# Kernel optimization log

Hardware: AMD Instinct MI355X
Metric: run time of the kernel (lower is better)

Reference implementation:

```python
import jax, jax.numpy as jnp
import numpy as np

H = 512          # hidden_size
SH = 120         # scoring_net_hidden_size
B = 1024         # batch
S = 64           # num_sentences


def setup_inputs() -> dict:
    key = jax.random.key(0)
    ks = jax.random.split(key, 12)
    sc = 0.05
    return {
        "C": jax.random.normal(ks[0], (B, S, H), jnp.float32),
        "Q": jax.random.normal(ks[1], (B, 1, H), jnp.float32),
        "prev_M": jax.random.normal(ks[2], (B, 1, H), jnp.float32),
        # scoring network params: fc1: 4H -> SH, fc2: SH -> 1
        "fc1_w": jax.random.normal(ks[3], (SH, 4 * H), jnp.float32) * sc,
        "fc1_b": jnp.zeros((SH,), jnp.float32),
        "fc2_w": jax.random.normal(ks[4], (1, SH), jnp.float32) * sc,
        "fc2_b": jnp.zeros((1,), jnp.float32),
        # GRU params (torch layout: rows ordered r, z, n)
        "W_ih": jax.random.normal(ks[5], (3 * H, H), jnp.float32) * sc,
        "W_hh": jax.random.normal(ks[6], (3 * H, H), jnp.float32) * sc,
        "b_ih": jnp.zeros((3 * H,), jnp.float32),
        "b_hh": jnp.zeros((3 * H,), jnp.float32),
    }


def reference(C, Q, prev_M, fc1_w, fc1_b, fc2_w, fc2_b, W_ih, W_hh, b_ih, b_hh):
    # --- scoring network (arch=1 feature vector) ---
    feat = jnp.concatenate(
        [C * Q, C * prev_M, jnp.abs(C - Q), jnp.abs(C - prev_M)], axis=2
    )  # [B, S, 4H]
    h1 = jnp.tanh(jnp.einsum("bsf,kf->bsk", feat, fc1_w) + fc1_b)
    G = jax.nn.sigmoid((jnp.einsum("bsk,ok->bso", h1, fc2_w) + fc2_b)[..., 0])  # [B, S]

    # --- gated GRU memory update over sentences ---
    xg_all = jnp.einsum("bsh,gh->bsg", C, W_ih) + b_ih  # [B, S, 3H] precomputed input gates

    def step(h, inp):
        xg, g = inp  # xg: [B, 3H], g: [B]
        hg = h @ W_hh.T + b_hh
        xr, xz, xn = jnp.split(xg, 3, axis=-1)
        hr, hz, hn = jnp.split(hg, 3, axis=-1)
        r = jax.nn.sigmoid(xr + hr)
        z = jax.nn.sigmoid(xz + hz)
        n = jnp.tanh(xn + r * hn)
        h_gru = (1.0 - z) * n + z * h          # standard torch GRU update
        g = g[:, None]
        h_new = g * h_gru + (1.0 - g) * h      # episodic gating
        return h_new, None

    h0 = jnp.zeros((C.shape[0], H), C.dtype)
    h_final, _ = jax.lax.scan(step, h0, (xg_all.transpose(1, 0, 2), G.T))
    return h_final[:, None, :]  # [B, 1, H]
```

## Files before the change

### kernel.cpp

```cpp
#include <hip/hip_runtime.h>
#include <hip/hip_bf16.h>

#define H_ 512
#define SH_ 120
#define B_ 1024
#define S_ 64

typedef __bf16 bf16x8 __attribute__((ext_vector_type(8)));
typedef float floatx4 __attribute__((ext_vector_type(4)));

__device__ __forceinline__ float bf2f(ushort u) {
    union { unsigned int i; float f; } v; v.i = ((unsigned int)u) << 16; return v.f;
}
__device__ __forceinline__ ushort f2bf(float f) {
    union { float f; unsigned int i; } v; v.f = f;
    unsigned int x = v.i;
    unsigned int r = (x + 0x7fffu + ((x >> 16) & 1u)) >> 16;
    return (ushort)r;
}

__global__ __launch_bounds__(256) void prep_w(
    const float* __restrict__ fc1w, ushort* __restrict__ fc1wb,
    const float* __restrict__ Wih,  ushort* __restrict__ Wihb,
    const float* __restrict__ Whh,  ushort* __restrict__ Whhb)
{
    const int stride = gridDim.x * blockDim.x;
    const int tid = blockIdx.x * blockDim.x + threadIdx.x;
    for (int i = tid; i < 61440; i += stride) {
        const float4 v = ((const float4*)fc1w)[i];
        ushort4 o; o.x = f2bf(v.x); o.y = f2bf(v.y); o.z = f2bf(v.z); o.w = f2bf(v.w);
        ((ushort4*)fc1wb)[i] = o;
    }
    for (int i = tid; i < 196608; i += stride) {
        const float4 v = ((const float4*)Wih)[i];
        ushort4 o; o.x = f2bf(v.x); o.y = f2bf(v.y); o.z = f2bf(v.z); o.w = f2bf(v.w);
        ((ushort4*)Wihb)[i] = o;
    }
    for (int i = tid; i < 196608; i += stride) {
        const float4 v = ((const float4*)Whh)[i];
        ushort4 o; o.x = f2bf(v.x); o.y = f2bf(v.y); o.z = f2bf(v.z); o.w = f2bf(v.w);
        ((ushort4*)Whhb)[i] = o;
    }
}

__global__ __launch_bounds__(256) void g_kernel(
    const float* __restrict__ C, const float* __restrict__ Q,
    const float* __restrict__ M, const ushort* __restrict__ fc1wb,
    const float* __restrict__ fc1b, const float* __restrict__ fc2w,
    const float* __restrict__ fc2b, float* __restrict__ G)
{
    __shared__ float qrow[H_];
    __shared__ float mrow[H_];
    __shared__ __align__(16) ushort featT[64 * 72];
    __shared__ __align__(16) ushort wT[128 * 72];
    __shared__ float h1s[64 * 132];

    const int b = blockIdx.x;
    const int t = threadIdx.x;
    for (int i = t; i < H_; i += 256) { qrow[i] = Q[(size_t)b * H_ + i]; mrow[i] = M[(size_t)b * H_ + i]; }

    const int wrow = t >> 1;
    const int wc0  = (t & 1) * 32;
    if (wrow >= SH_) {
        uint4* dst = (uint4*)&wT[wrow * 72 + wc0];
        const uint4 z = {0u, 0u, 0u, 0u};
        dst[0] = z; dst[1] = z; dst[2] = z; dst[3] = z;
    }
    __syncthreads();

    const int lane = t & 63;
    const int wv   = t >> 6;
    const int quad = lane >> 4;
    const int l15  = lane & 15;
    const int arow = wv * 16 + l15;
    const int s    = t >> 2;
    const int c0   = (t & 3) * 16;

    floatx4 acc[8];
#pragma unroll
    for (int i = 0; i < 8; ++i) acc[i] = (floatx4){0.f, 0.f, 0.f, 0.f};

    for (int hc = 0; hc < H_; hc += 64) {
        float cr[16];
        {
            const float4* csrc = (const float4*)(C + ((size_t)b * S_ + s) * H_ + hc + c0);
            *(float4*)&cr[0]  = csrc[0];
            *(float4*)&cr[4]  = csrc[1];
            *(float4*)&cr[8]  = csrc[2];
            *(float4*)&cr[12] = csrc[3];
        }
#pragma unroll
        for (int seg = 0; seg < 4; ++seg) {
#pragma unroll
            for (int u = 0; u < 16; ++u) {
                const int kk = c0 + u;
                const float c = cr[u];
                const float o = (seg == 0 || seg == 2) ? qrow[hc + kk] : mrow[hc + kk];
                const float v = (seg < 2) ? c * o : fabsf(c - o);
                featT[s * 72 + kk] = f2bf(v);
            }
            if (wrow < SH_) {
                const uint4* src = (const uint4*)(fc1wb + (size_t)wrow * (4 * H_) + seg * H_ + hc + wc0);
                uint4* dst = (uint4*)&wT[wrow * 72 + wc0];
                dst[0] = src[0]; dst[1] = src[1]; dst[2] = src[2]; dst[3] = src[3];
            }
            __syncthreads();
#pragma unroll
            for (int ks = 0; ks < 64; ks += 32) {
                const int ao = ks + quad * 8;
                const bf16x8 af = *(const bf16x8*)&featT[arow * 72 + ao];
#pragma unroll
                for (int nt = 0; nt < 8; ++nt) {
                    const bf16x8 bfr = *(const bf16x8*)&wT[(nt * 16 + l15) * 72 + ao];
                    acc[nt] = __builtin_amdgcn_mfma_f32_16x16x32_bf16(af, bfr, acc[nt], 0, 0, 0);
                }
            }
            __syncthreads();
        }
    }

#pragma unroll
    for (int nt = 0; nt < 8; ++nt) {
        const int col = nt * 16 + l15;
        const float bias = (col < SH_) ? fc1b[col] : 0.f;
#pragma unroll
        for (int r = 0; r < 4; ++r) {
            const int row = wv * 16 + quad * 4 + r;
            h1s[row * 132 + col] = (col < SH_) ? tanhf(acc[nt][r] + bias) : 0.f;
        }
    }
    __syncthreads();
    {
        const int part = t & 3;
        float sum = 0.f;
        for (int k = part; k < SH_; k += 4) sum += h1s[s * 132 + k] * fc2w[k];
        sum += __shfl_xor(sum, 1);
        sum += __shfl_xor(sum, 2);
        if (part == 0) {
            const float logit = sum + fc2b[0];
            G[(size_t)b * S_ + s] = 1.f / (1.f + expf(-logit));
        }
    }
}

__global__ __launch_bounds__(256) void scan_step(
    const float* __restrict__ C, const ushort* __restrict__ Wihb,
    const ushort* __restrict__ Whhb, const float* __restrict__ bih,
    const float* __restrict__ bhh, const float* __restrict__ G,
    const ushort* __restrict__ hhi_r, const ushort* __restrict__ hlo_r,
    ushort* __restrict__ hhi_w, ushort* __restrict__ hlo_w,
    float* __restrict__ out, int tstep, int last)
{
    __shared__ __align__(16) ushort As[3 * 4608];
    __shared__ __align__(16) ushort Bs[2 * 6912];

    const int bx = blockIdx.x;
    const int jt = bx & 15;
    const int bt = bx >> 4;
    const int jb = jt * 32;
    const int bb = bt * 64;
    const int t  = threadIdx.x;
    const int lane = t & 63;
    const int wv   = t >> 6;
    const int quad = lane >> 4;
    const int l15  = lane & 15;
    const int arow = wv * 16 + l15;
    const int crow = t >> 2;
    const int cc0  = (t & 3) * 16;

    floatx4 acc_r[2], acc_z[2], acc_xn[2], acc_hn[2];
#pragma unroll
    for (int i = 0; i < 2; ++i) {
        acc_r[i] = (floatx4){0.f,0.f,0.f,0.f}; acc_z[i]  = (floatx4){0.f,0.f,0.f,0.f};
        acc_xn[i]= (floatx4){0.f,0.f,0.f,0.f}; acc_hn[i] = (floatx4){0.f,0.f,0.f,0.f};
    }

    for (int kc = 0; kc < H_; kc += 64) {
        {
            const float4* src = (const float4*)(C + ((size_t)(bb + crow) * S_ + tstep) * H_ + kc + cc0);
            float cr[16];
            *(float4*)&cr[0]  = src[0];
            *(float4*)&cr[4]  = src[1];
            *(float4*)&cr[8]  = src[2];
            *(float4*)&cr[12] = src[3];
            __align__(16) ushort cb[16];
#pragma unroll
            for (int u = 0; u < 16; ++u) cb[u] = f2bf(cr[u]);
            uint4* d = (uint4*)&As[crow * 72 + cc0];
            d[0] = ((uint4*)cb)[0]; d[1] = ((uint4*)cb)[1];
        }
#pragma unroll
        for (int i = 0; i < 4; ++i) {
            const int gid  = i * 256 + t;
            const int tile = gid >> 9;
            const int rem  = gid & 511;
            const int row  = rem >> 3;
            const int grp  = rem & 7;
            const ushort* src = (tile ? hlo_r : hhi_r) + (size_t)(bb + row) * H_ + kc + grp * 8;
            *(uint4*)&As[(1 + tile) * 4608 + row * 72 + grp * 8] = *(const uint4*)src;
        }
#pragma unroll
        for (int i = 0; i < 6; ++i) {
            const int gid = i * 256 + t;
            const int mat = (gid >= 768) ? 1 : 0;
            const int rem = gid - mat * 768;
            const int row = rem >> 3;
            const int grp = rem & 7;
            const int gate = row >> 5;
            const int jj   = row & 31;
            const int grow = gate * H_ + jb + jj;
            const ushort* src = (mat ? Whhb : Wihb) + (size_t)grow * H_ + kc + grp * 8;
            *(uint4*)&Bs[mat * 6912 + row * 72 + grp * 8] = *(const uint4*)src;
        }
        __syncthreads();
#pragma unroll
        for (int ks = 0; ks < 64; ks += 32) {
            const int ao = ks + quad * 8;
            const bf16x8 a_c  = *(const bf16x8*)&As[0 * 4608 + arow * 72 + ao];
            const bf16x8 a_hh = *(const bf16x8*)&As[1 * 4608 + arow * 72 + ao];
            const bf16x8 a_hl = *(const bf16x8*)&As[2 * 4608 + arow * 72 + ao];
#pragma unroll
            for (int nt = 0; nt < 2; ++nt) {
                const int jj = nt * 16 + l15;
                const bf16x8 ih_r = *(const bf16x8*)&Bs[0 * 6912 + (0 * 32 + jj) * 72 + ao];
                const bf16x8 ih_z = *(const bf16x8*)&Bs[0 * 6912 + (1 * 32 + jj) * 72 + ao];
                const bf16x8 ih_n = *(const bf16x8*)&Bs[0 * 6912 + (2 * 32 + jj) * 72 + ao];
                const bf16x8 hh_r = *(const bf16x8*)&Bs[1 * 6912 + (0 * 32 + jj) * 72 + ao];
                const bf16x8 hh_z = *(const bf16x8*)&Bs[1 * 6912 + (1 * 32 + jj) * 72 + ao];
                const bf16x8 hh_n = *(const bf16x8*)&Bs[1 * 6912 + (2 * 32 + jj) * 72 + ao];
                acc_r[nt]  = __builtin_amdgcn_mfma_f32_16x16x32_bf16(a_c,  ih_r, acc_r[nt],  0, 0, 0);
                acc_r[nt]  = __builtin_amdgcn_mfma_f32_16x16x32_bf16(a_hh, hh_r, acc_r[nt],  0, 0, 0);
                acc_r[nt]  = __builtin_amdgcn_mfma_f32_16x16x32_bf16(a_hl, hh_r, acc_r[nt],  0, 0, 0);
                acc_z[nt]  = __builtin_amdgcn_mfma_f32_16x16x32_bf16(a_c,  ih_z, acc_z[nt],  0, 0, 0);
                acc_z[nt]  = __builtin_amdgcn_mfma_f32_16x16x32_bf16(a_hh, hh_z, acc_z[nt],  0, 0, 0);
                acc_z[nt]  = __builtin_amdgcn_mfma_f32_16x16x32_bf16(a_hl, hh_z, acc_z[nt],  0, 0, 0);
                acc_xn[nt] = __builtin_amdgcn_mfma_f32_16x16x32_bf16(a_c,  ih_n, acc_xn[nt], 0, 0, 0);
                acc_hn[nt] = __builtin_amdgcn_mfma_f32_16x16x32_bf16(a_hh, hh_n, acc_hn[nt], 0, 0, 0);
                acc_hn[nt] = __builtin_amdgcn_mfma_f32_16x16x32_bf16(a_hl, hh_n, acc_hn[nt], 0, 0, 0);
            }
        }
        __syncthreads();
    }

#pragma unroll
    for (int nt = 0; nt < 2; ++nt) {
        const int j = jb + nt * 16 + l15;
        const float br  = bih[j]          + bhh[j];
        const float bz  = bih[H_ + j]     + bhh[H_ + j];
        const float bxn = bih[2 * H_ + j];
        const float bhn = bhh[2 * H_ + j];
#pragma unroll
        for (int r4 = 0; r4 < 4; ++r4) {
            const int b = bb + wv * 16 + quad * 4 + r4;
            const size_t idx = (size_t)b * H_ + j;
            const float hold = bf2f(hhi_r[idx]) + bf2f(hlo_r[idx]);
            const float g = G[(size_t)b * S_ + tstep];
            const float rg = 1.f / (1.f + expf(-(acc_r[nt][r4] + br)));
            const float zg = 1.f / (1.f + expf(-(acc_z[nt][r4] + bz)));
            const float ng = tanhf(acc_xn[nt][r4] + bxn + rg * (acc_hn[nt][r4] + bhn));
            const float hgru = (1.f - zg) * ng + zg * hold;
            const float hnew = g * hgru + (1.f - g) * hold;
            const ushort hb = f2bf(hnew);
            hhi_w[idx] = hb;
            hlo_w[idx] = f2bf(hnew - bf2f(hb));
            if (last) out[idx] = hnew;
        }
    }
}

extern "C" void kernel_launch(void* const* d_in, const int* in_sizes, int n_in,
                              void* d_out, int out_size, void* d_ws, size_t ws_size,
                              hipStream_t stream) {
    (void)in_sizes; (void)n_in; (void)out_size; (void)ws_size;
    const float* C    = (const float*)d_in[0];
    const float* Q    = (const float*)d_in[1];
    const float* M    = (const float*)d_in[2];
    const float* fc1w = (const float*)d_in[3];
    const float* fc1b = (const float*)d_in[4];
    const float* fc2w = (const float*)d_in[5];
    const float* fc2b = (const float*)d_in[6];
    const float* Wih  = (const float*)d_in[7];
    const float* Whh  = (const float*)d_in[8];
    const float* bih  = (const float*)d_in[9];
    const float* bhh  = (const float*)d_in[10];
    float* out = (float*)d_out;

    char* ws = (char*)d_ws;
    float*  Gbuf  = (float*)ws;
    ushort* hhi0  = (ushort*)(ws + 262144);
    ushort* hlo0  = (ushort*)(ws + 262144 + 1048576);
    ushort* hhi1  = (ushort*)(ws + 262144 + 2097152);
    ushort* hlo1  = (ushort*)(ws + 262144 + 3145728);
    ushort* fc1wb = (ushort*)(ws + 4456448);
    ushort* Wihb  = (ushort*)(ws + 4947968);
    ushort* Whhb  = (ushort*)(ws + 6520832);

    hipMemsetAsync(hhi0, 0, 2097152, stream);

    prep_w<<<256, 256, 0, stream>>>(fc1w, fc1wb, Wih, Wihb, Whh, Whhb);
    g_kernel<<<B_, 256, 0, stream>>>(C, Q, M, fc1wb, fc1b, fc2w, fc2b, Gbuf);
    for (int t = 0; t < S_; ++t) {
        const ushort* hr_hi = (t & 1) ? hhi1 : hhi0;
        const ushort* hr_lo = (t & 1) ? hlo1 : hlo0;
        ushort* hw_hi = (t & 1) ? hhi0 : hhi1;
        ushort* hw_lo = (t & 1) ? hlo0 : hlo1;
        scan_step<<<256, 256, 0, stream>>>(C, Wihb, Whhb, bih, bhh, Gbuf,
                                           hr_hi, hr_lo, hw_hi, hw_lo,
                                           out, t, (t == S_ - 1) ? 1 : 0);
    }
}
```

Baseline: 1.462 ms.

## Hoist input-gate GEMM out of scan into chunked batched xg kernel

The input projection C·W_ih moves out of each per-step scan kernel into a separate batched GEMM kernel. That kernel computes bf16 xg for 8 timesteps at a time using 128x256 tiles with double-buffered LDS. The scan step now only does the recurrent W_hh matmul over the split-precision hidden state, with register-prefetched double buffering, and reads the precomputed xg from a workspace buffer. This removes the redundant per-step W_ih loads and small-tile inefficiency, but adds xg global traffic, an extra bf16 rounding of the input gates, and 8 more launches.

```diff
diff --git a/kernel.cpp b/kernel.cpp
--- a/kernel.cpp
+++ b/kernel.cpp
@@ -17,6 +17,10 @@
     unsigned int x = v.i;
     unsigned int r = (x + 0x7fffu + ((x >> 16) & 1u)) >> 16;
     return (ushort)r;
+}
+__device__ __forceinline__ ushort f2bf_fast(float f) {
+    __bf16 b = (__bf16)f;
+    union { __bf16 b; ushort u; } v; v.b = b; return v.u;
 }
 
 __global__ __launch_bounds__(256) void prep_w(
@@ -143,16 +147,111 @@
     }
 }
 
-__global__ __launch_bounds__(256) void scan_step(
+__global__ __launch_bounds__(256, 1) void xg_kernel(
     const float* __restrict__ C, const ushort* __restrict__ Wihb,
-    const ushort* __restrict__ Whhb, const float* __restrict__ bih,
-    const float* __restrict__ bhh, const float* __restrict__ G,
+    ushort* __restrict__ xg, int c)
+{
+    __shared__ __align__(16) ushort As[2][128 * 72];
+    __shared__ __align__(16) ushort Bs[2][256 * 72];
+
+    const int bx = blockIdx.x;
+    const int mt = bx & 63;
+    const int ntile = bx >> 6;
+    const int t = threadIdx.x;
+    const int lane = t & 63;
+    const int wv   = t >> 6;
+    const int quad = lane >> 4;
+    const int l15  = lane & 15;
+
+    const int ar = t >> 1;
+    const int ah = (t & 1) * 32;
+    const int grow = mt * 128 + ar;
+    const float* aptr = C + ((size_t)(grow >> 3) * S_ + c * 8 + (grow & 7)) * H_ + ah;
+    const ushort* bptr = Wihb + (size_t)(ntile * 256 + t) * H_;
+
+    floatx4 acc[2][16];
+#pragma unroll
+    for (int i = 0; i < 2; ++i)
+#pragma unroll
+        for (int j = 0; j < 16; ++j) acc[i][j] = (floatx4){0.f, 0.f, 0.f, 0.f};
+
+    {
+        float av[32];
+#pragma unroll
+        for (int q = 0; q < 8; ++q) *(float4*)&av[q * 4] = *(const float4*)(aptr + q * 4);
+        __align__(16) ushort ab[32];
+#pragma unroll
+        for (int u = 0; u < 32; ++u) ab[u] = f2bf_fast(av[u]);
+        uint4* dst = (uint4*)&As[0][ar * 72 + ah];
+        dst[0] = ((uint4*)ab)[0]; dst[1] = ((uint4*)ab)[1];
+        dst[2] = ((uint4*)ab)[2]; dst[3] = ((uint4*)ab)[3];
+#pragma unroll
+        for (int g = 0; g < 8; ++g)
+            *(uint4*)&Bs[0][t * 72 + g * 8] = *(const uint4*)(bptr + g * 8);
+    }
+    __syncthreads();
+
+    for (int kci = 0; kci < 8; ++kci) {
+        const int cur = kci & 1;
+        float av[32]; uint4 bv[8];
+        if (kci < 7) {
+            const int kn = (kci + 1) * 64;
+#pragma unroll
+            for (int q = 0; q < 8; ++q) *(float4*)&av[q * 4] = *(const float4*)(aptr + kn + q * 4);
+#pragma unroll
+            for (int g = 0; g < 8; ++g) bv[g] = *(const uint4*)(bptr + kn + g * 8);
+        }
+#pragma unroll
+        for (int ks = 0; ks < 64; ks += 32) {
+            const int ao = ks + quad * 8;
+            const bf16x8 a0 = *(const bf16x8*)&As[cur][(wv * 32 + l15) * 72 + ao];
+            const bf16x8 a1 = *(const bf16x8*)&As[cur][(wv * 32 + 16 + l15) * 72 + ao];
+#pragma unroll
+            for (int nf = 0; nf < 16; ++nf) {
+                const bf16x8 bfr = *(const bf16x8*)&Bs[cur][(nf * 16 + l15) * 72 + ao];
+                acc[0][nf] = __builtin_amdgcn_mfma_f32_16x16x32_bf16(a0, bfr, acc[0][nf], 0, 0, 0);
+                acc[1][nf] = __builtin_amdgcn_mfma_f32_16x16x32_bf16(a1, bfr, acc[1][nf], 0, 0, 0);
+            }
+        }
+        if (kci < 7) {
+            __align__(16) ushort ab[32];
+#pragma unroll
+            for (int u = 0; u < 32; ++u) ab[u] = f2bf_fast(av[u]);
+            uint4* dst = (uint4*)&As[cur ^ 1][ar * 72 + ah];
+            dst[0] = ((uint4*)ab)[0]; dst[1] = ((uint4*)ab)[1];
+            dst[2] = ((uint4*)ab)[2]; dst[3] = ((uint4*)ab)[3];
+#pragma unroll
+            for (int g = 0; g < 8; ++g)
+                *(uint4*)&Bs[cur ^ 1][t * 72 + g * 8] = bv[g];
+        }
+        __syncthreads();
+    }
+
+#pragma unroll
+    for (int mf = 0; mf < 2; ++mf) {
+#pragma unroll
+        for (int nf = 0; nf < 16; ++nf) {
+            const int n = ntile * 256 + nf * 16 + l15;
+#pragma unroll
+            for (int r = 0; r < 4; ++r) {
+                const int row = mt * 128 + wv * 32 + mf * 16 + quad * 4 + r;
+                xg[(size_t)row * 1536 + n] = f2bf(acc[mf][nf][r]);
+            }
+        }
+    }
+}
+
+__global__ __launch_bounds__(256, 1) void scan_step(
+    const ushort* __restrict__ xg, const ushort* __restrict__ Whhb,
+    const float* __restrict__ bih, const float* __restrict__ bhh,
+    const float* __restrict__ G,
     const ushort* __restrict__ hhi_r, const ushort* __restrict__ hlo_r,
     ushort* __restrict__ hhi_w, ushort* __restrict__ hlo_w,
-    float* __restrict__ out, int tstep, int last)
+    float* __restrict__ out, int tstep, int sl, int last)
 {
-    __shared__ __align__(16) ushort As[3 * 4608];
-    __shared__ __align__(16) ushort Bs[2 * 6912];
+    __shared__ __align__(16) ushort Hs[2][2 * 4608];
+    __shared__ __align__(16) ushort Ws[2][6912];
+    __shared__ __align__(16) ushort xgs[64 * 96];
 
     const int bx = blockIdx.x;
     const int jt = bx & 15;
@@ -165,30 +264,25 @@
     const int quad = lane >> 4;
     const int l15  = lane & 15;
     const int arow = wv * 16 + l15;
-    const int crow = t >> 2;
-    const int cc0  = (t & 3) * 16;
-
-    floatx4 acc_r[2], acc_z[2], acc_xn[2], acc_hn[2];
+
+    floatx4 acc_r[2], acc_z[2], acc_xn2[2], acc_hn[2];
 #pragma unroll
     for (int i = 0; i < 2; ++i) {
-        acc_r[i] = (floatx4){0.f,0.f,0.f,0.f}; acc_z[i]  = (floatx4){0.f,0.f,0.f,0.f};
-        acc_xn[i]= (floatx4){0.f,0.f,0.f,0.f}; acc_hn[i] = (floatx4){0.f,0.f,0.f,0.f};
-    }
-
-    for (int kc = 0; kc < H_; kc += 64) {
-        {
-            const float4* src = (const float4*)(C + ((size_t)(bb + crow) * S_ + tstep) * H_ + kc + cc0);
-            float cr[16];
-            *(float4*)&cr[0]  = src[0];
-            *(float4*)&cr[4]  = src[1];
-            *(float4*)&cr[8]  = src[2];
-            *(float4*)&cr[12] = src[3];
-            __align__(16) ushort cb[16];
-#pragma unroll
-            for (int u = 0; u < 16; ++u) cb[u] = f2bf(cr[u]);
-            uint4* d = (uint4*)&As[crow * 72 + cc0];
-            d[0] = ((uint4*)cb)[0]; d[1] = ((uint4*)cb)[1];
-        }
+        acc_r[i] = (floatx4){0.f,0.f,0.f,0.f}; acc_z[i]   = (floatx4){0.f,0.f,0.f,0.f};
+        acc_xn2[i]=(floatx4){0.f,0.f,0.f,0.f}; acc_hn[i]  = (floatx4){0.f,0.f,0.f,0.f};
+    }
+
+#pragma unroll
+    for (int i = 0; i < 3; ++i) {
+        const int gid  = i * 256 + t;
+        const int seg  = gid >> 2;
+        const int q    = gid & 3;
+        const int row  = seg / 3;
+        const int gate = seg - row * 3;
+        const ushort* src = xg + ((size_t)(bb + row) * 8 + sl) * 1536 + gate * H_ + jb + q * 8;
+        *(uint4*)&xgs[row * 96 + gate * 32 + q * 8] = *(const uint4*)src;
+    }
+    {
 #pragma unroll
         for (int i = 0; i < 4; ++i) {
             const int gid  = i * 256 + t;
@@ -196,47 +290,83 @@
             const int rem  = gid & 511;
             const int row  = rem >> 3;
             const int grp  = rem & 7;
-            const ushort* src = (tile ? hlo_r : hhi_r) + (size_t)(bb + row) * H_ + kc + grp * 8;
-            *(uint4*)&As[(1 + tile) * 4608 + row * 72 + grp * 8] = *(const uint4*)src;
-        }
-#pragma unroll
-        for (int i = 0; i < 6; ++i) {
+            const ushort* src = (tile ? hlo_r : hhi_r) + (size_t)(bb + row) * H_ + grp * 8;
+            *(uint4*)&Hs[0][tile * 4608 + row * 72 + grp * 8] = *(const uint4*)src;
+        }
+#pragma unroll
+        for (int i = 0; i < 3; ++i) {
             const int gid = i * 256 + t;
-            const int mat = (gid >= 768) ? 1 : 0;
-            const int rem = gid - mat * 768;
-            const int row = rem >> 3;
-            const int grp = rem & 7;
+            const int row = gid >> 3;
+            const int grp = gid & 7;
             const int gate = row >> 5;
             const int jj   = row & 31;
-            const int grow = gate * H_ + jb + jj;
-            const ushort* src = (mat ? Whhb : Wihb) + (size_t)grow * H_ + kc + grp * 8;
-            *(uint4*)&Bs[mat * 6912 + row * 72 + grp * 8] = *(const uint4*)src;
-        }
-        __syncthreads();
+            const ushort* src = Whhb + (size_t)(gate * H_ + jb + jj) * H_ + grp * 8;
+            *(uint4*)&Ws[0][row * 72 + grp * 8] = *(const uint4*)src;
+        }
+    }
+    __syncthreads();
+
+    for (int kci = 0; kci < 8; ++kci) {
+        const int cur = kci & 1;
+        uint4 hv[4], wvr[3];
+        if (kci < 7) {
+            const int kn = (kci + 1) * 64;
+#pragma unroll
+            for (int i = 0; i < 4; ++i) {
+                const int gid  = i * 256 + t;
+                const int tile = gid >> 9;
+                const int rem  = gid & 511;
+                const int row  = rem >> 3;
+                const int grp  = rem & 7;
+                const ushort* src = (tile ? hlo_r : hhi_r) + (size_t)(bb + row) * H_ + kn + grp * 8;
+                hv[i] = *(const uint4*)src;
+            }
+#pragma unroll
+            for (int i = 0; i < 3; ++i) {
+                const int gid = i * 256 + t;
+                const int row = gid >> 3;
+                const int grp = gid & 7;
+                const int gate = row >> 5;
+                const int jj   = row & 31;
+                wvr[i] = *(const uint4*)(Whhb + (size_t)(gate * H_ + jb + jj) * H_ + kn + grp * 8);
+            }
+        }
 #pragma unroll
         for (int ks = 0; ks < 64; ks += 32) {
             const int ao = ks + quad * 8;
-            const bf16x8 a_c  = *(const bf16x8*)&As[0 * 4608 + arow * 72 + ao];
-            const bf16x8 a_hh = *(const bf16x8*)&As[1 * 4608 + arow * 72 + ao];
-            const bf16x8 a_hl = *(const bf16x8*)&As[2 * 4608 + arow * 72 + ao];
+            const bf16x8 a_hh = *(const bf16x8*)&Hs[cur][arow * 72 + ao];
+            const bf16x8 a_hl = *(const bf16x8*)&Hs[cur][4608 + arow * 72 + ao];
 #pragma unroll
             for (int nt = 0; nt < 2; ++nt) {
                 const int jj = nt * 16 + l15;
-                const bf16x8 ih_r = *(const bf16x8*)&Bs[0 * 6912 + (0 * 32 + jj) * 72 + ao];
-                const bf16x8 ih_z = *(const bf16x8*)&Bs[0 * 6912 + (1 * 32 + jj) * 72 + ao];
-                const bf16x8 ih_n = *(const bf16x8*)&Bs[0 * 6912 + (2 * 32 + jj) * 72 + ao];
-                const bf16x8 hh_r = *(const bf16x8*)&Bs[1 * 6912 + (0 * 32 + jj) * 72 + ao];
-                const bf16x8 hh_z = *(const bf16x8*)&Bs[1 * 6912 + (1 * 32 + jj) * 72 + ao];
-                const bf16x8 hh_n = *(const bf16x8*)&Bs[1 * 6912 + (2 * 32 + jj) * 72 + ao];
-                acc_r[nt]  = __builtin_amdgcn_mfma_f32_16x16x32_bf16(a_c,  ih_r, acc_r[nt],  0, 0, 0);
-                acc_r[nt]  = __builtin_amdgcn_mfma_f32_16x16x32_bf16(a_hh, hh_r, acc_r[nt],  0, 0, 0);
-                acc_r[nt]  = __builtin_amdgcn_mfma_f32_16x16x32_bf16(a_hl, hh_r, acc_r[nt],  0, 0, 0);
-                acc_z[nt]  = __builtin_amdgcn_mfma_f32_16x16x32_bf16(a_c,  ih_z, acc_z[nt],  0, 0, 0);
-                acc_z[nt]  = __builtin_amdgcn_mfma_f32_16x16x32_bf16(a_hh, hh_z, acc_z[nt],  0, 0, 0);
-                acc_z[nt]  = __builtin_amdgcn_mfma_f32_16x16x32_bf16(a_hl, hh_z, acc_z[nt],  0, 0, 0);
-                acc_xn[nt] = __builtin_amdgcn_mfma_f32_16x16x32_bf16(a_c,  ih_n, acc_xn[nt], 0, 0, 0);
-                acc_hn[nt] = __builtin_amdgcn_mfma_f32_16x16x32_bf16(a_hh, hh_n, acc_hn[nt], 0, 0, 0);
-                acc_hn[nt] = __builtin_amdgcn_mfma_f32_16x16x32_bf16(a_hl, hh_n, acc_hn[nt], 0, 0, 0);
+                const bf16x8 w_r = *(const bf16x8*)&Ws[cur][(0 * 32 + jj) * 72 + ao];
+                const bf16x8 w_z = *(const bf16x8*)&Ws[cur][(1 * 32 + jj) * 72 + ao];
+                const bf16x8 w_n = *(const bf16x8*)&Ws[cur][(2 * 32 + jj) * 72 + ao];
+                acc_r[nt]  = __builtin_amdgcn_mfma_f32_16x16x32_bf16(a_hh, w_r, acc_r[nt],  0, 0, 0);
+                acc_r[nt]  = __builtin_amdgcn_mfma_f32_16x16x32_bf16(a_hl, w_r, acc_r[nt],  0, 0, 0);
+                acc_z[nt]  = __builtin_amdgcn_mfma_f32_16x16x32_bf16(a_hh, w_z, acc_z[nt],  0, 0, 0);
+                acc_z[nt]  = __builtin_amdgcn_mfma_f32_16x16x32_bf16(a_hl, w_z, acc_z[nt],  0, 0, 0);
+                acc_hn[nt] = __builtin_amdgcn_mfma_f32_16x16x32_bf16(a_hh, w_n, acc_hn[nt], 0, 0, 0);
+                acc_hn[nt] = __builtin_amdgcn_mfma_f32_16x16x32_bf16(a_hl, w_n, acc_hn[nt], 0, 0, 0);
+            }
+        }
+        if (kci < 7) {
+            const int cn = cur ^ 1;
+#pragma unroll
+            for (int i = 0; i < 4; ++i) {
+                const int gid  = i * 256 + t;
+                const int tile = gid >> 9;
+                const int rem  = gid & 511;
+                const int row  = rem >> 3;
+                const int grp  = rem & 7;
+                *(uint4*)&Hs[cn][tile * 4608 + row * 72 + grp * 8] = hv[i];
+            }
+#pragma unroll
+            for (int i = 0; i < 3; ++i) {
+                const int gid = i * 256 + t;
+                const int row = gid >> 3;
+                const int grp = gid & 7;
+                *(uint4*)&Ws[cn][row * 72 + grp * 8] = wvr[i];
             }
         }
         __syncthreads();
@@ -244,20 +374,25 @@
 
 #pragma unroll
     for (int nt = 0; nt < 2; ++nt) {
-        const int j = jb + nt * 16 + l15;
+        const int jc = nt * 16 + l15;
+        const int j  = jb + jc;
         const float br  = bih[j]          + bhh[j];
         const float bz  = bih[H_ + j]     + bhh[H_ + j];
         const float bxn = bih[2 * H_ + j];
         const float bhn = bhh[2 * H_ + j];
 #pragma unroll
         for (int r4 = 0; r4 < 4; ++r4) {
-            const int b = bb + wv * 16 + quad * 4 + r4;
+            const int bl = wv * 16 + quad * 4 + r4;
+            const int b  = bb + bl;
             const size_t idx = (size_t)b * H_ + j;
+            const float xr = bf2f(xgs[bl * 96 + 0 * 32 + jc]);
+            const float xz = bf2f(xgs[bl * 96 + 1 * 32 + jc]);
+            const float xn = bf2f(xgs[bl * 96 + 2 * 32 + jc]);
             const float hold = bf2f(hhi_r[idx]) + bf2f(hlo_r[idx]);
             const float g = G[(size_t)b * S_ + tstep];
-            const float rg = 1.f / (1.f + expf(-(acc_r[nt][r4] + br)));
-            const float zg = 1.f / (1.f + expf(-(acc_z[nt][r4] + bz)));
-            const float ng = tanhf(acc_xn[nt][r4] + bxn + rg * (acc_hn[nt][r4] + bhn));
+            const float rg = 1.f / (1.f + expf(-(acc_r[nt][r4] + xr + br)));
+            const float zg = 1.f / (1.f + expf(-(acc_z[nt][r4] + xz + bz)));
+            const float ng = tanhf(xn + bxn + rg * (acc_hn[nt][r4] + bhn));
             const float hgru = (1.f - zg) * ng + zg * hold;
             const float hnew = g * hgru + (1.f - g) * hold;
             const ushort hb = f2bf(hnew);
@@ -294,18 +429,24 @@
     ushort* fc1wb = (ushort*)(ws + 4456448);
     ushort* Wihb  = (ushort*)(ws + 4947968);
     ushort* Whhb  = (ushort*)(ws + 6520832);
+    ushort* xgbuf = (ushort*)(ws + 8093696);
 
     hipMemsetAsync(hhi0, 0, 2097152, stream);
 
     prep_w<<<256, 256, 0, stream>>>(fc1w, fc1wb, Wih, Wihb, Whh, Whhb);
     g_kernel<<<B_, 256, 0, stream>>>(C, Q, M, fc1wb, fc1b, fc2w, fc2b, Gbuf);
-    for (int t = 0; t < S_; ++t) {
-        const ushort* hr_hi = (t & 1) ? hhi1 : hhi0;
-        const ushort* hr_lo = (t & 1) ? hlo1 : hlo0;
-        ushort* hw_hi = (t & 1) ? hhi0 : hhi1;
-        ushort* hw_lo = (t & 1) ? hlo0 : hlo1;
-        scan_step<<<256, 256, 0, stream>>>(C, Wihb, Whhb, bih, bhh, Gbuf,
-                                           hr_hi, hr_lo, hw_hi, hw_lo,
-                                           out, t, (t == S_ - 1) ? 1 : 0);
-    }
-}
+
+    for (int c = 0; c < 8; ++c) {
+        xg_kernel<<<384, 256, 0, stream>>>(C, Wihb, xgbuf, c);
+        for (int sl = 0; sl < 8; ++sl) {
+            const int tt = c * 8 + sl;
+            const ushort* hr_hi = (tt & 1) ? hhi1 : hhi0;
+            const ushort* hr_lo = (tt & 1) ? hlo1 : hlo0;
+            ushort* hw_hi = (tt & 1) ? hhi0 : hhi1;
+            ushort* hw_lo = (tt & 1) ? hlo0 : hlo1;
+            scan_step<<<256, 256, 0, stream>>>(xgbuf, Whhb, bih, bhh, Gbuf,
+                                               hr_hi, hr_lo, hw_hi, hw_lo,
+                                               out, tt, sl, (tt == S_ - 1) ? 1 : 0);
+        }
+    }
+}
```

Measured after the change: 1.620 ms. 10.8% more time.

## Replace per-step scan launches with persistent kernel holding W_hh in LDS

Applied to the files above, without the earlier changes.

The 64 per-timestep launches are replaced by one persistent kernel of 256 blocks. Each block keeps its W_hh slice resident in LDS and precomputes the input-gate projections for chunks of 8 timesteps into a workspace buffer. Blocks sharing a batch tile synchronise each step through a global atomic counter barrier, and the recurrent h loads are double-buffered. This removes launch overhead and the repeated W_hh and W_ih reloads, but it needs about 156 KB of LDS per block and depends on all blocks being co-resident for the spin barrier to avoid deadlock.

```diff
diff --git a/kernel.cpp b/kernel.cpp
--- a/kernel.cpp
+++ b/kernel.cpp
@@ -143,127 +143,221 @@
     }
 }
 
-__global__ __launch_bounds__(256) void scan_step(
+__global__ __launch_bounds__(256) void persist(
     const float* __restrict__ C, const ushort* __restrict__ Wihb,
     const ushort* __restrict__ Whhb, const float* __restrict__ bih,
     const float* __restrict__ bhh, const float* __restrict__ G,
-    const ushort* __restrict__ hhi_r, const ushort* __restrict__ hlo_r,
-    ushort* __restrict__ hhi_w, ushort* __restrict__ hlo_w,
-    float* __restrict__ out, int tstep, int last)
+    ushort* __restrict__ xgw,
+    ushort* __restrict__ hhi0, ushort* __restrict__ hlo0,
+    ushort* __restrict__ hhi1, ushort* __restrict__ hlo1,
+    unsigned* __restrict__ ctr, float* __restrict__ out)
 {
-    __shared__ __align__(16) ushort As[3 * 4608];
-    __shared__ __align__(16) ushort Bs[2 * 6912];
-
-    const int bx = blockIdx.x;
-    const int jt = bx & 15;
-    const int bt = bx >> 4;
-    const int jb = jt * 32;
-    const int bb = bt * 64;
-    const int t  = threadIdx.x;
+    extern __shared__ __align__(16) ushort smem[];
+    ushort* WhhL = smem;
+    ushort* Hb   = smem + 55296;
+    ushort* Xs   = smem + 55296 + 18432;
+
+    const int bx  = blockIdx.x;
+    const int bt  = (bx & 7) * 2 + (bx >> 7);
+    const int jt  = (bx & 127) >> 3;
+    const int jb  = jt * 32;
+    const int bb  = bt * 64;
+    const int t   = threadIdx.x;
     const int lane = t & 63;
     const int wv   = t >> 6;
     const int quad = lane >> 4;
     const int l15  = lane & 15;
     const int arow = wv * 16 + l15;
-    const int crow = t >> 2;
-    const int cc0  = (t & 3) * 16;
-
-    floatx4 acc_r[2], acc_z[2], acc_xn[2], acc_hn[2];
-#pragma unroll
-    for (int i = 0; i < 2; ++i) {
-        acc_r[i] = (floatx4){0.f,0.f,0.f,0.f}; acc_z[i]  = (floatx4){0.f,0.f,0.f,0.f};
-        acc_xn[i]= (floatx4){0.f,0.f,0.f,0.f}; acc_hn[i] = (floatx4){0.f,0.f,0.f,0.f};
-    }
-
-    for (int kc = 0; kc < H_; kc += 64) {
-        {
-            const float4* src = (const float4*)(C + ((size_t)(bb + crow) * S_ + tstep) * H_ + kc + cc0);
-            float cr[16];
-            *(float4*)&cr[0]  = src[0];
-            *(float4*)&cr[4]  = src[1];
-            *(float4*)&cr[8]  = src[2];
-            *(float4*)&cr[12] = src[3];
-            __align__(16) ushort cb[16];
-#pragma unroll
-            for (int u = 0; u < 16; ++u) cb[u] = f2bf(cr[u]);
-            uint4* d = (uint4*)&As[crow * 72 + cc0];
-            d[0] = ((uint4*)cb)[0]; d[1] = ((uint4*)cb)[1];
-        }
-#pragma unroll
-        for (int i = 0; i < 4; ++i) {
-            const int gid  = i * 256 + t;
-            const int tile = gid >> 9;
-            const int rem  = gid & 511;
-            const int row  = rem >> 3;
-            const int grp  = rem & 7;
-            const ushort* src = (tile ? hlo_r : hhi_r) + (size_t)(bb + row) * H_ + kc + grp * 8;
-            *(uint4*)&As[(1 + tile) * 4608 + row * 72 + grp * 8] = *(const uint4*)src;
-        }
-#pragma unroll
-        for (int i = 0; i < 6; ++i) {
-            const int gid = i * 256 + t;
-            const int mat = (gid >= 768) ? 1 : 0;
-            const int rem = gid - mat * 768;
-            const int row = rem >> 3;
-            const int grp = rem & 7;
-            const int gate = row >> 5;
-            const int jj   = row & 31;
-            const int grow = gate * H_ + jb + jj;
-            const ushort* src = (mat ? Whhb : Wihb) + (size_t)grow * H_ + kc + grp * 8;
-            *(uint4*)&Bs[mat * 6912 + row * 72 + grp * 8] = *(const uint4*)src;
-        }
+    ushort* __restrict__ xgp = xgw + (size_t)bx * 49152;
+
+    for (int kci = 0; kci < 8; ++kci) {
+#pragma unroll
+        for (int i = 0; i < 3; ++i) {
+            const int gidx = i * 256 + t;
+            const int row = gidx >> 3, grp = gidx & 7;
+            const int gate = row >> 5, jj = row & 31;
+            *(uint4*)&WhhL[kci * 6912 + row * 72 + grp * 8] =
+                *(const uint4*)(Whhb + (size_t)(gate * H_ + jb + jj) * H_ + kci * 64 + grp * 8);
+        }
+    }
+    __syncthreads();
+
+    for (int c = 0; c < 8; ++c) {
+        for (int sub = 0; sub < 8; ++sub) {
+            floatx4 xacc[6];
+#pragma unroll
+            for (int i = 0; i < 6; ++i) xacc[i] = (floatx4){0.f, 0.f, 0.f, 0.f};
+            for (int kci = 0; kci < 8; ++kci) {
+                {
+                    const int arw = t >> 2;
+                    const int ac0 = (t & 3) * 16;
+                    const int m = sub * 64 + arw;
+                    const float4* src = (const float4*)(C +
+                        ((size_t)(bb + (m >> 3)) * S_ + c * 8 + (m & 7)) * H_ + kci * 64 + ac0);
+                    float cr[16];
+                    *(float4*)&cr[0]  = src[0];
+                    *(float4*)&cr[4]  = src[1];
+                    *(float4*)&cr[8]  = src[2];
+                    *(float4*)&cr[12] = src[3];
+                    __align__(16) ushort cb[16];
+#pragma unroll
+                    for (int u = 0; u < 16; ++u) cb[u] = f2bf(cr[u]);
+                    uint4* d = (uint4*)&Xs[arw * 72 + ac0];
+                    d[0] = ((uint4*)cb)[0]; d[1] = ((uint4*)cb)[1];
+                }
+#pragma unroll
+                for (int i = 0; i < 3; ++i) {
+                    const int gidx = i * 256 + t;
+                    const int row = gidx >> 3, grp = gidx & 7;
+                    const int gate = row >> 5, jj = row & 31;
+                    *(uint4*)&Hb[row * 72 + grp * 8] =
+                        *(const uint4*)(Wihb + (size_t)(gate * H_ + jb + jj) * H_ + kci * 64 + grp * 8);
+                }
+                __syncthreads();
+#pragma unroll
+                for (int ks = 0; ks < 64; ks += 32) {
+                    const int ao = ks + quad * 8;
+                    const bf16x8 af = *(const bf16x8*)&Xs[arow * 72 + ao];
+#pragma unroll
+                    for (int nf = 0; nf < 6; ++nf) {
+                        const bf16x8 bw = *(const bf16x8*)&Hb[(nf * 16 + l15) * 72 + ao];
+                        xacc[nf] = __builtin_amdgcn_mfma_f32_16x16x32_bf16(af, bw, xacc[nf], 0, 0, 0);
+                    }
+                }
+                __syncthreads();
+            }
+#pragma unroll
+            for (int nf = 0; nf < 6; ++nf) {
+#pragma unroll
+                for (int r = 0; r < 4; ++r) {
+                    const int m = sub * 64 + wv * 16 + quad * 4 + r;
+                    xgp[m * 96 + nf * 16 + l15] = f2bf(xacc[nf][r]);
+                }
+            }
+        }
+        __threadfence();
         __syncthreads();
-#pragma unroll
-        for (int ks = 0; ks < 64; ks += 32) {
-            const int ao = ks + quad * 8;
-            const bf16x8 a_c  = *(const bf16x8*)&As[0 * 4608 + arow * 72 + ao];
-            const bf16x8 a_hh = *(const bf16x8*)&As[1 * 4608 + arow * 72 + ao];
-            const bf16x8 a_hl = *(const bf16x8*)&As[2 * 4608 + arow * 72 + ao];
+
+        for (int sl = 0; sl < 8; ++sl) {
+            const int tstep = c * 8 + sl;
+            const ushort* __restrict__ hhi_r = (tstep & 1) ? hhi1 : hhi0;
+            const ushort* __restrict__ hlo_r = (tstep & 1) ? hlo1 : hlo0;
+            ushort* __restrict__ hhi_w = (tstep & 1) ? hhi0 : hhi1;
+            ushort* __restrict__ hlo_w = (tstep & 1) ? hlo0 : hlo1;
+
+            floatx4 acc_r[2], acc_z[2], acc_hn[2];
+#pragma unroll
+            for (int i = 0; i < 2; ++i) {
+                acc_r[i] = (floatx4){0.f,0.f,0.f,0.f};
+                acc_z[i] = (floatx4){0.f,0.f,0.f,0.f};
+                acc_hn[i]= (floatx4){0.f,0.f,0.f,0.f};
+            }
+
+#pragma unroll
+            for (int i = 0; i < 3; ++i) {
+                const int gid = i * 256 + t;
+                const int row = gid / 12;
+                const int q   = gid - row * 12;
+                *(uint4*)&Xs[row * 96 + q * 8] =
+                    *(const uint4*)(xgp + (row * 8 + sl) * 96 + q * 8);
+            }
+#pragma unroll
+            for (int i = 0; i < 4; ++i) {
+                const int gid  = i * 256 + t;
+                const int tile = gid >> 9;
+                const int rem  = gid & 511;
+                const int row  = rem >> 3, grp = rem & 7;
+                *(uint4*)&Hb[tile * 4608 + row * 72 + grp * 8] =
+                    *(const uint4*)((tile ? hlo_r : hhi_r) + (size_t)(bb + row) * H_ + grp * 8);
+            }
+            __syncthreads();
+
+            for (int kci = 0; kci < 8; ++kci) {
+                const int cur = kci & 1;
+                uint4 hv[4];
+                if (kci < 7) {
+                    const int kn = (kci + 1) * 64;
+#pragma unroll
+                    for (int i = 0; i < 4; ++i) {
+                        const int gid  = i * 256 + t;
+                        const int tile = gid >> 9;
+                        const int rem  = gid & 511;
+                        const int row  = rem >> 3, grp = rem & 7;
+                        hv[i] = *(const uint4*)((tile ? hlo_r : hhi_r) + (size_t)(bb + row) * H_ + kn + grp * 8);
+                    }
+                }
+#pragma unroll
+                for (int ks = 0; ks < 64; ks += 32) {
+                    const int ao = ks + quad * 8;
+                    const bf16x8 a_hh = *(const bf16x8*)&Hb[cur * 9216 + arow * 72 + ao];
+                    const bf16x8 a_hl = *(const bf16x8*)&Hb[cur * 9216 + 4608 + arow * 72 + ao];
+#pragma unroll
+                    for (int nt = 0; nt < 2; ++nt) {
+                        const int jj = nt * 16 + l15;
+                        const bf16x8 w_r = *(const bf16x8*)&WhhL[kci * 6912 + (0 * 32 + jj) * 72 + ao];
+                        const bf16x8 w_z = *(const bf16x8*)&WhhL[kci * 6912 + (1 * 32 + jj) * 72 + ao];
+                        const bf16x8 w_n = *(const bf16x8*)&WhhL[kci * 6912 + (2 * 32 + jj) * 72 + ao];
+                        acc_r[nt]  = __builtin_amdgcn_mfma_f32_16x16x32_bf16(a_hh, w_r, acc_r[nt],  0, 0, 0);
+                        acc_r[nt]  = __builtin_amdgcn_mfma_f32_16x16x32_bf16(a_hl, w_r, acc_r[nt],  0, 0, 0);
+                        acc_z[nt]  = __builtin_amdgcn_mfma_f32_16x16x32_bf16(a_hh, w_z, acc_z[nt],  0, 0, 0);
+                        acc_z[nt]  = __builtin_amdgcn_mfma_f32_16x16x32_bf16(a_hl, w_z, acc_z[nt],  0, 0, 0);
+                        acc_hn[nt] = __builtin_amdgcn_mfma_f32_16x16x32_bf16(a_hh, w_n, acc_hn[nt], 0, 0, 0);
+                        acc_hn[nt] = __builtin_amdgcn_mfma_f32_16x16x32_bf16(a_hl, w_n, acc_hn[nt], 0, 0, 0);
+                    }
+                }
+                if (kci < 7) {
+                    const int cn = cur ^ 1;
+#pragma unroll
+                    for (int i = 0; i < 4; ++i) {
+                        const int gid  = i * 256 + t;
+                        const int tile = gid >> 9;
+                        const int rem  = gid & 511;
+                        const int row  = rem >> 3, grp = rem & 7;
+                        *(uint4*)&Hb[cn * 9216 + tile * 4608 + row * 72 + grp * 8] = hv[i];
+                    }
+                }
+                __syncthreads();
+            }
+
 #pragma unroll
             for (int nt = 0; nt < 2; ++nt) {
-                const int jj = nt * 16 + l15;
-                const bf16x8 ih_r = *(const bf16x8*)&Bs[0 * 6912 + (0 * 32 + jj) * 72 + ao];
-                const bf16x8 ih_z = *(const bf16x8*)&Bs[0 * 6912 + (1 * 32 + jj) * 72 + ao];
-                const bf16x8 ih_n = *(const bf16x8*)&Bs[0 * 6912 + (2 * 32 + jj) * 72 + ao];
-                const bf16x8 hh_r = *(const bf16x8*)&Bs[1 * 6912 + (0 * 32 + jj) * 72 + ao];
-                const bf16x8 hh_z = *(const bf16x8*)&Bs[1 * 6912 + (1 * 32 + jj) * 72 + ao];
-                const bf16x8 hh_n = *(const bf16x8*)&Bs[1 * 6912 + (2 * 32 + jj) * 72 + ao];
-                acc_r[nt]  = __builtin_amdgcn_mfma_f32_16x16x32_bf16(a_c,  ih_r, acc_r[nt],  0, 0, 0);
-                acc_r[nt]  = __builtin_amdgcn_mfma_f32_16x16x32_bf16(a_hh, hh_r, acc_r[nt],  0, 0, 0);
-                acc_r[nt]  = __builtin_amdgcn_mfma_f32_16x16x32_bf16(a_hl, hh_r, acc_r[nt],  0, 0, 0);
-                acc_z[nt]  = __builtin_amdgcn_mfma_f32_16x16x32_bf16(a_c,  ih_z, acc_z[nt],  0, 0, 0);
-                acc_z[nt]  = __builtin_amdgcn_mfma_f32_16x16x32_bf16(a_hh, hh_z, acc_z[nt],  0, 0, 0);
-                acc_z[nt]  = __builtin_amdgcn_mfma_f32_16x16x32_bf16(a_hl, hh_z, acc_z[nt],  0, 0, 0);
-                acc_xn[nt] = __builtin_amdgcn_mfma_f32_16x16x32_bf16(a_c,  ih_n, acc_xn[nt], 0, 0, 0);
-                acc_hn[nt] = __builtin_amdgcn_mfma_f32_16x16x32_bf16(a_hh, hh_n, acc_hn[nt], 0, 0, 0);
-                acc_hn[nt] = __builtin_amdgcn_mfma_f32_16x16x32_bf16(a_hl, hh_n, acc_hn[nt], 0, 0, 0);
-            }
-        }
-        __syncthreads();
-    }
-
-#pragma unroll
-    for (int nt = 0; nt < 2; ++nt) {
-        const int j = jb + nt * 16 + l15;
-        const float br  = bih[j]          + bhh[j];
-        const float bz  = bih[H_ + j]     + bhh[H_ + j];
-        const float bxn = bih[2 * H_ + j];
-        const float bhn = bhh[2 * H_ + j];
-#pragma unroll
-        for (int r4 = 0; r4 < 4; ++r4) {
-            const int b = bb + wv * 16 + quad * 4 + r4;
-            const size_t idx = (size_t)b * H_ + j;
-            const float hold = bf2f(hhi_r[idx]) + bf2f(hlo_r[idx]);
-            const float g = G[(size_t)b * S_ + tstep];
-            const float rg = 1.f / (1.f + expf(-(acc_r[nt][r4] + br)));
-            const float zg = 1.f / (1.f + expf(-(acc_z[nt][r4] + bz)));
-            const float ng = tanhf(acc_xn[nt][r4] + bxn + rg * (acc_hn[nt][r4] + bhn));
-            const float hgru = (1.f - zg) * ng + zg * hold;
-            const float hnew = g * hgru + (1.f - g) * hold;
-            const ushort hb = f2bf(hnew);
-            hhi_w[idx] = hb;
-            hlo_w[idx] = f2bf(hnew - bf2f(hb));
-            if (last) out[idx] = hnew;
+                const int jc = nt * 16 + l15;
+                const int j  = jb + jc;
+                const float br  = bih[j]          + bhh[j];
+                const float bz  = bih[H_ + j]     + bhh[H_ + j];
+                const float bxn = bih[2 * H_ + j] + 0.f;
+                const float bhn = bhh[2 * H_ + j];
+#pragma unroll
+                for (int r4 = 0; r4 < 4; ++r4) {
+                    const int bl = wv * 16 + quad * 4 + r4;
+                    const int b  = bb + bl;
+                    const size_t idx = (size_t)b * H_ + j;
+                    const float xr = bf2f(Xs[bl * 96 + 0 * 32 + jc]);
+                    const float xz = bf2f(Xs[bl * 96 + 1 * 32 + jc]);
+                    const float xn = bf2f(Xs[bl * 96 + 2 * 32 + jc]);
+                    const float hold = bf2f(hhi_r[idx]) + bf2f(hlo_r[idx]);
+                    const float g = G[(size_t)b * S_ + tstep];
+                    const float rg = 1.f / (1.f + expf(-(acc_r[nt][r4] + xr + br)));
+                    const float zg = 1.f / (1.f + expf(-(acc_z[nt][r4] + xz + bz)));
+                    const float ng = tanhf(xn + bxn + rg * (acc_hn[nt][r4] + bhn));
+                    const float hgru = (1.f - zg) * ng + zg * hold;
+                    const float hnew = g * hgru + (1.f - g) * hold;
+                    const ushort hb = f2bf(hnew);
+                    hhi_w[idx] = hb;
+                    hlo_w[idx] = f2bf(hnew - bf2f(hb));
+                    if (tstep == S_ - 1) out[idx] = hnew;
+                }
+            }
+
+            __threadfence();
+            __syncthreads();
+            if (t == 0) {
+                atomicAdd(ctr + bt, 1u);
+                const unsigned target = 16u * (unsigned)(tstep + 1);
+                while (atomicAdd(ctr + bt, 0u) < target) __builtin_amdgcn_s_sleep(2);
+            }
+            __syncthreads();
+            __threadfence();
         }
     }
 }
@@ -286,26 +380,30 @@
     float* out = (float*)d_out;
 
     char* ws = (char*)d_ws;
-    float*  Gbuf  = (float*)ws;
-    ushort* hhi0  = (ushort*)(ws + 262144);
-    ushort* hlo0  = (ushort*)(ws + 262144 + 1048576);
-    ushort* hhi1  = (ushort*)(ws + 262144 + 2097152);
-    ushort* hlo1  = (ushort*)(ws + 262144 + 3145728);
-    ushort* fc1wb = (ushort*)(ws + 4456448);
-    ushort* Wihb  = (ushort*)(ws + 4947968);
-    ushort* Whhb  = (ushort*)(ws + 6520832);
+    float*    Gbuf  = (float*)ws;
+    ushort*   hhi0  = (ushort*)(ws + 262144);
+    ushort*   hlo0  = (ushort*)(ws + 262144 + 1048576);
+    ushort*   hhi1  = (ushort*)(ws + 262144 + 2097152);
+    ushort*   hlo1  = (ushort*)(ws + 262144 + 3145728);
+    ushort*   fc1wb = (ushort*)(ws + 4456448);
+    ushort*   Wihb  = (ushort*)(ws + 4947968);
+    ushort*   Whhb  = (ushort*)(ws + 6520832);
+    ushort*   xgw   = (ushort*)(ws + 8093696);
+    unsigned* ctr   = (unsigned*)(ws + 8093696 + 25165824);
 
     hipMemsetAsync(hhi0, 0, 2097152, stream);
+    hipMemsetAsync(ctr, 0, 64, stream);
 
     prep_w<<<256, 256, 0, stream>>>(fc1w, fc1wb, Wih, Wihb, Whh, Whhb);
     g_kernel<<<B_, 256, 0, stream>>>(C, Q, M, fc1wb, fc1b, fc2w, fc2b, Gbuf);
-    for (int t = 0; t < S_; ++t) {
-        const ushort* hr_hi = (t & 1) ? hhi1 : hhi0;
-        const ushort* hr_lo = (t & 1) ? hlo1 : hlo0;
-        ushort* hw_hi = (t & 1) ? hhi0 : hhi1;
-        ushort* hw_lo = (t & 1) ? hlo0 : hlo1;
-        scan_step<<<256, 256, 0, stream>>>(C, Wihb, Whhb, bih, bhh, Gbuf,
-                                           hr_hi, hr_lo, hw_hi, hw_lo,
-                                           out, t, (t == S_ - 1) ? 1 : 0);
-    }
-}
+
+    const int lds_bytes = 159744;
+    static bool attr_set = false;
+    if (!attr_set) {
+        hipFuncSetAttribute((const void*)persist,
+                            hipFuncAttributeMaxDynamicSharedMemorySize, 160 * 1024);
+        attr_set = true;
+    }
+    persist<<<256, 256, lds_bytes, stream>>>(C, Wihb, Whhb, bih, bhh, Gbuf,
+                                             xgw, hhi0, hlo0, hhi1, hlo1, ctr, out);
+}
```

New measurement: 4.247 ms. 2.91x slower.
